# Kernel tuning notes

Measured on AMD Instinct MI355X. Metric: run time of the kernel, lower is better.

## Reference

```python
import jax, jax.numpy as jnp
import numpy as np

N_NODES = 50000
N_EDGES = 600000
DIMS = [128, 128, 128]  # input_dim + hidden_dims


def setup_inputs() -> dict:
    key = jax.random.key(0)
    ks = jax.random.split(key, 8)
    node_features = jax.random.normal(ks[0], (N_NODES, DIMS[0]), dtype=jnp.float32)
    edge_index = jax.random.randint(ks[1], (2, N_EDGES), 0, N_NODES, dtype=jnp.int64)
    # GCNConv params: weight [in, out] (glorot-ish), bias [out] (zeros init in PyG; use small randn)
    W1 = jax.random.normal(ks[2], (DIMS[0], DIMS[1]), dtype=jnp.float32) / np.sqrt(DIMS[0])
    b1 = jnp.zeros((DIMS[1],), dtype=jnp.float32)
    W2 = jax.random.normal(ks[3], (DIMS[1], DIMS[2]), dtype=jnp.float32) / np.sqrt(DIMS[1])
    b2 = jnp.zeros((DIMS[2],), dtype=jnp.float32)
    return {"node_features": node_features, "edge_index": edge_index,
            "W1": W1, "b1": b1, "W2": W2, "b2": b2}


def _gcn_norm(edge_index, n_nodes):
    # Add self loops, then symmetric normalization as in PyG gcn_norm.
    loop = jnp.arange(n_nodes, dtype=edge_index.dtype)
    src = jnp.concatenate([edge_index[0], loop])  # message sources (x_j)
    dst = jnp.concatenate([edge_index[1], loop])  # aggregation targets
    deg = jax.ops.segment_sum(jnp.ones_like(dst, dtype=jnp.float32), dst,
                              num_segments=n_nodes)
    dinv = jnp.where(deg > 0, jax.lax.rsqrt(jnp.maximum(deg, 1.0)), 0.0)
    norm = dinv[src] * dinv[dst]  # [E + N]
    return src, dst, norm


def _gcn_layer(x, W, b, src, dst, norm, n_nodes):
    h = x @ W                                  # [N, out]
    msgs = h[src] * norm[:, None]              # gather + scale  [E+N, out]
    out = jax.ops.segment_sum(msgs, dst, num_segments=n_nodes)  # scatter-add
    return out + b


def reference(node_features, edge_index, W1, b1, W2, b2):
    n_nodes = node_features.shape[0]
    src, dst, norm = _gcn_norm(edge_index, n_nodes)
    x = _gcn_layer(node_features, W1, b1, src, dst, norm, n_nodes)
    x = jax.nn.relu(x)  # ReLU between layers, none after last
    x = _gcn_layer(x, W2, b2, src, dst, norm, n_nodes)
    return x
```

## Files before the change

### kernel.cpp

```cpp
#include <hip/hip_runtime.h>
#include <hip/hip_bf16.h>

typedef __bf16 bf16_t;
typedef __bf16 bf16x8 __attribute__((ext_vector_type(8)));
typedef float f32x4 __attribute__((ext_vector_type(4)));
typedef unsigned short u16;

#define DIM 128
#define CAPE 62

__global__ void k_prep(const float* __restrict__ W1, const float* __restrict__ W2,
                       bf16_t* __restrict__ TH1, bf16_t* __restrict__ TL1,
                       bf16_t* __restrict__ TH2, bf16_t* __restrict__ TL2) {
    int b = blockIdx.x;
    const float* W = (b == 0) ? W1 : W2;
    bf16_t* TH = (b == 0) ? TH1 : TH2;
    bf16_t* TL = (b == 0) ? TL1 : TL2;
    for (int idx = threadIdx.x; idx < 128 * 128; idx += 256) {
        int j    = idx & 7;
        int lane = (idx >> 3) & 63;
        int kc   = (idx >> 9) & 3;
        int nt   = idx >> 11;
        int nn = nt * 16 + (lane & 15);
        int k  = kc * 32 + (lane >> 4) * 8 + j;
        float wv = W[k * 128 + nn];
        bf16_t h = (bf16_t)wv;
        TH[idx] = h;
        TL[idx] = (bf16_t)(wv - (float)h);
    }
}

__global__ __launch_bounds__(256) void k_front(
        const bf16_t* __restrict__ TH1, const bf16_t* __restrict__ TL1,
        const float* __restrict__ A, bf16_t* __restrict__ H, int M, int SB,
        const int* __restrict__ EI, int* __restrict__ ell, int e) {
    int b = blockIdx.x;
    int tid = threadIdx.x;
    if (b < SB) {
        __shared__ int any;
        if (tid == 0) any = 0;
        __syncthreads();
        long e0 = ((long)b * 256 + tid) * 8;
        long rem = (long)e - e0;
        int ns = rem >= 8 ? 8 : (rem > 0 ? (int)rem : 0);
        int s[8], d[8];
        int hi = 0;
        if (ns == 8) {
            int4 p0 = *(const int4*)(EI + 2 * e0);
            int4 p1 = *(const int4*)(EI + 2 * e0 + 4);
            int4 p2 = *(const int4*)(EI + 2 * e0 + 8);
            int4 p3 = *(const int4*)(EI + 2 * e0 + 12);
            s[0] = p0.x; s[1] = p0.z; s[2] = p1.x; s[3] = p1.z;
            s[4] = p2.x; s[5] = p2.z; s[6] = p3.x; s[7] = p3.z;
            hi = (p0.y | p0.w) | (p1.y | p1.w) | (p2.y | p2.w) | (p3.y | p3.w);
        } else {
            for (int q = 0; q < 8; q++) s[q] = 0;
            for (int q = 0; q < ns; q++) { s[q] = EI[2 * (e0 + q)]; hi |= EI[2 * (e0 + q) + 1]; }
        }
        if (hi) atomicOr(&any, 1);
        __syncthreads();
        for (int q = 0; q < 8; q++) d[q] = 0;
        if (any == 0) {
            if (ns == 8) {
                int4 q0 = *(const int4*)(EI + 2 * ((long)e + e0));
                int4 q1 = *(const int4*)(EI + 2 * ((long)e + e0) + 4);
                int4 q2 = *(const int4*)(EI + 2 * ((long)e + e0) + 8);
                int4 q3 = *(const int4*)(EI + 2 * ((long)e + e0) + 12);
                d[0] = q0.x; d[1] = q0.z; d[2] = q1.x; d[3] = q1.z;
                d[4] = q2.x; d[5] = q2.z; d[6] = q3.x; d[7] = q3.z;
            } else {
                for (int q = 0; q < ns; q++) d[q] = EI[2 * ((long)e + e0 + q)];
            }
        } else {
            if (ns == 8) {
                int4 s0 = *(const int4*)(EI + e0);
                int4 s1 = *(const int4*)(EI + e0 + 4);
                s[0] = s0.x; s[1] = s0.y; s[2] = s0.z; s[3] = s0.w;
                s[4] = s1.x; s[5] = s1.y; s[6] = s1.z; s[7] = s1.w;
                int4 d0 = *(const int4*)(EI + (long)e + e0);
                int4 d1 = *(const int4*)(EI + (long)e + e0 + 4);
                d[0] = d0.x; d[1] = d0.y; d[2] = d0.z; d[3] = d0.w;
                d[4] = d1.x; d[5] = d1.y; d[6] = d1.z; d[7] = d1.w;
            } else {
                for (int q = 0; q < ns; q++) { s[q] = EI[e0 + q]; d[q] = EI[(long)e + e0 + q]; }
            }
        }
        int pos[8];
#pragma unroll
        for (int q = 0; q < 8; q++)
            if (q < ns) pos[q] = atomicAdd(ell + (long)d[q] * 32 + 31, 1);
#pragma unroll
        for (int q = 0; q < 8; q++)
            if (q < ns && pos[q] < CAPE)
                ((u16*)ell)[(long)d[q] * 64 + pos[q]] = (u16)s[q];
        return;
    }
    int wave = tid >> 6, lane = tid & 63;
    long row_base = ((long)(b - SB) * 4 + wave) * 16;
    if (row_base >= M) return;
    int n16 = lane & 15, quad = lane >> 4;

    bf16x8 a_hi[4], a_lo[4];
    const float* arow = A + (row_base + n16) * DIM + quad * 8;
#pragma unroll
    for (int kc = 0; kc < 4; kc++) {
        float4 p0 = *(const float4*)(arow + kc * 32);
        float4 p1 = *(const float4*)(arow + kc * 32 + 4);
        float v[8] = {p0.x, p0.y, p0.z, p0.w, p1.x, p1.y, p1.z, p1.w};
#pragma unroll
        for (int j = 0; j < 8; j++) {
            bf16_t h = (bf16_t)v[j];
            a_hi[kc][j] = h;
            a_lo[kc][j] = (bf16_t)(v[j] - (float)h);
        }
    }
#pragma unroll
    for (int nt = 0; nt < 8; nt++) {
        f32x4 acc = {0.f, 0.f, 0.f, 0.f};
#pragma unroll
        for (int kc = 0; kc < 4; kc++) {
            long tb = ((long)(nt * 4 + kc) * 64 + lane) * 8;
            bf16x8 bh = *(const bf16x8*)(TH1 + tb);
            bf16x8 bl = *(const bf16x8*)(TL1 + tb);
            acc = __builtin_amdgcn_mfma_f32_16x16x32_bf16(a_hi[kc], bh, acc, 0, 0, 0);
            acc = __builtin_amdgcn_mfma_f32_16x16x32_bf16(a_lo[kc], bh, acc, 0, 0, 0);
            acc = __builtin_amdgcn_mfma_f32_16x16x32_bf16(a_hi[kc], bl, acc, 0, 0, 0);
        }
        bf16_t* hrow = H + (row_base + quad * 4) * DIM + nt * 16 + n16;
#pragma unroll
        for (int r = 0; r < 4; r++) hrow[(long)r * DIM] = (bf16_t)acc[r];
    }
}

__global__ void k_dinv(const int* __restrict__ ell, float* __restrict__ dinv, int n) {
    int g = blockIdx.x * 256 + threadIdx.x;
    if (g < n) dinv[g] = rsqrtf((float)(ell[(long)g * 32 + 31] + 1));
}

__global__ __launch_bounds__(256) void k_aggemm(const bf16_t* __restrict__ H,
        const int* __restrict__ ell, const float* __restrict__ dinv,
        const float* __restrict__ bias,
        const bf16_t* __restrict__ TH, const bf16_t* __restrict__ TL,
        bf16_t* __restrict__ H2, int n) {
    __shared__ bf16_t tile[16 * 128];
    __shared__ float sdinv[16];
    int lane = threadIdx.x & 63;
    int wave = threadIdx.x >> 6;
    int sub = lane >> 4;
    int sl  = lane & 15;
    int lr  = wave * 4 + sub;
    long i  = (long)blockIdx.x * 16 + lr;

    float d = dinv[i];
    int deg = ell[i * 32 + 31];
    if (deg > CAPE) deg = CAPE;
    const u16* crow = (const u16*)(ell + i * 32);
    float acc[8];
    {
        bf16x8 hs = *(const bf16x8*)(H + i * DIM + sl * 8);
#pragma unroll
        for (int q = 0; q < 8; q++) acc[q] = d * (float)hs[q];
    }
    ushort4 c0 = ((const ushort4*)crow)[0];
    ushort4 c1 = ((const ushort4*)crow)[1];
    ushort4 c2 = ((const ushort4*)crow)[2];
    ushort4 c3 = ((const ushort4*)crow)[3];
    u16 cols[16] = {c0.x, c0.y, c0.z, c0.w, c1.x, c1.y, c1.z, c1.w,
                    c2.x, c2.y, c2.z, c2.w, c3.x, c3.y, c3.z, c3.w};
    bf16x8 hv[16];
    float wv[16];
#pragma unroll
    for (int j = 0; j < 16; j++)
        if (j < deg) {
            int s0 = cols[j];
            wv[j] = dinv[s0];
            hv[j] = *(const bf16x8*)(H + (long)s0 * DIM + sl * 8);
        }
#pragma unroll
    for (int j = 0; j < 16; j++)
        if (j < deg) {
#pragma unroll
            for (int q = 0; q < 8; q++) acc[q] += wv[j] * (float)hv[j][q];
        }
    for (int j = 16; j < deg; j++) {
        int s0 = crow[j];
        float w0 = dinv[s0];
        bf16x8 h0 = *(const bf16x8*)(H + (long)s0 * DIM + sl * 8);
#pragma unroll
        for (int q = 0; q < 8; q++) acc[q] += w0 * (float)h0[q];
    }
    {
        float4 b0 = *(const float4*)(bias + sl * 8);
        float4 b1 = *(const float4*)(bias + sl * 8 + 4);
        float r[8];
        r[0] = d * acc[0] + b0.x; r[1] = d * acc[1] + b0.y;
        r[2] = d * acc[2] + b0.z; r[3] = d * acc[3] + b0.w;
        r[4] = d * acc[4] + b1.x; r[5] = d * acc[5] + b1.y;
        r[6] = d * acc[6] + b1.z; r[7] = d * acc[7] + b1.w;
        bf16x8 o;
#pragma unroll
        for (int q = 0; q < 8; q++) o[q] = (bf16_t)fmaxf(r[q], 0.f);
        int off = lr * 256 + ((sl * 16) ^ ((lr & 7) << 4));
        *(bf16x8*)((char*)tile + off) = o;
        if (sl == 0) sdinv[lr] = d;
    }
    __syncthreads();

    int n16 = sl, quad = sub;
    bf16x8 a[4];
#pragma unroll
    for (int kc = 0; kc < 4; kc++) {
        int off = n16 * 256 + (((kc * 64 + quad * 16)) ^ ((n16 & 7) << 4));
        a[kc] = *(const bf16x8*)((char*)tile + off);
    }
    float dr[4];
#pragma unroll
    for (int r = 0; r < 4; r++) dr[r] = sdinv[quad * 4 + r];
    long row_base = (long)blockIdx.x * 16;
#pragma unroll
    for (int t = 0; t < 2; t++) {
        int nt = wave * 2 + t;
        f32x4 acc2 = {0.f, 0.f, 0.f, 0.f};
#pragma unroll
        for (int kc = 0; kc < 4; kc++) {
            long tb = ((long)(nt * 4 + kc) * 64 + lane) * 8;
            bf16x8 bh = *(const bf16x8*)(TH + tb);
            bf16x8 bl = *(const bf16x8*)(TL + tb);
            acc2 = __builtin_amdgcn_mfma_f32_16x16x32_bf16(a[kc], bh, acc2, 0, 0, 0);
            acc2 = __builtin_amdgcn_mfma_f32_16x16x32_bf16(a[kc], bl, acc2, 0, 0, 0);
        }
        bf16_t* hrow = H2 + (row_base + quad * 4) * DIM + nt * 16 + n16;
#pragma unroll
        for (int r = 0; r < 4; r++) hrow[(long)r * DIM] = (bf16_t)(dr[r] * acc2[r]);
    }
}

__global__ __launch_bounds__(256) void k_agg2(const bf16_t* __restrict__ H,
        const int* __restrict__ ell, const float* __restrict__ dinv,
        const float* __restrict__ bias, float* __restrict__ outf, int n) {
    int lane = threadIdx.x & 63;
    int wave = threadIdx.x >> 6;
    int sub = lane >> 4;
    int sl  = lane & 15;
    long i = (long)(blockIdx.x * 4 + wave) * 4 + sub;
    if (i >= n) return;
    float d = dinv[i];
    int deg = ell[i * 32 + 31];
    if (deg > CAPE) deg = CAPE;
    const u16* crow = (const u16*)(ell + i * 32);
    float acc[8];
    {
        bf16x8 hs = *(const bf16x8*)(H + i * DIM + sl * 8);
#pragma unroll
        for (int q = 0; q < 8; q++) acc[q] = (float)hs[q];
    }
    ushort4 c0 = ((const ushort4*)crow)[0];
    ushort4 c1 = ((const ushort4*)crow)[1];
    ushort4 c2 = ((const ushort4*)crow)[2];
    ushort4 c3 = ((const ushort4*)crow)[3];
    u16 cols[16] = {c0.x, c0.y, c0.z, c0.w, c1.x, c1.y, c1.z, c1.w,
                    c2.x, c2.y, c2.z, c2.w, c3.x, c3.y, c3.z, c3.w};
    bf16x8 hv[16];
#pragma unroll
    for (int j = 0; j < 16; j++)
        if (j < deg) hv[j] = *(const bf16x8*)(H + (long)cols[j] * DIM + sl * 8);
#pragma unroll
    for (int j = 0; j < 16; j++)
        if (j < deg) {
#pragma unroll
            for (int q = 0; q < 8; q++) acc[q] += (float)hv[j][q];
        }
    for (int j = 16; j < deg; j++) {
        int s0 = crow[j];
        bf16x8 h0 = *(const bf16x8*)(H + (long)s0 * DIM + sl * 8);
#pragma unroll
        for (int q = 0; q < 8; q++) acc[q] += (float)h0[q];
    }
    {
        float4 b0 = *(const float4*)(bias + sl * 8);
        float4 b1 = *(const float4*)(bias + sl * 8 + 4);
        float* op = outf + i * DIM + sl * 8;
        *(float4*)op = make_float4(d * acc[0] + b0.x, d * acc[1] + b0.y,
                                   d * acc[2] + b0.z, d * acc[3] + b0.w);
        *(float4*)(op + 4) = make_float4(d * acc[4] + b1.x, d * acc[5] + b1.y,
                                         d * acc[6] + b1.z, d * acc[7] + b1.w);
    }
}

extern "C" void kernel_launch(void* const* d_in, const int* in_sizes, int n_in,
                              void* d_out, int out_size, void* d_ws, size_t ws_size,
                              hipStream_t stream) {
    const float* X  = (const float*)d_in[0];
    const int*   EI = (const int*)d_in[1];
    const float* W1 = (const float*)d_in[2];
    const float* B1 = (const float*)d_in[3];
    const float* W2 = (const float*)d_in[4];
    const float* B2 = (const float*)d_in[5];
    float* OUT = (float*)d_out;

    const int N = in_sizes[0] / DIM;
    const int E = in_sizes[1] / 2;
    (void)n_in; (void)out_size; (void)ws_size;

    char* w = (char*)d_ws;
    auto alloc = [&](size_t bytes) -> char* {
        char* p = w;
        w += (bytes + 255) & ~(size_t)255;
        return p;
    };
    int*    ell  = (int*)alloc((size_t)N * 128);
    float*  dinv = (float*)alloc((size_t)N * 4);
    bf16_t* TH1  = (bf16_t*)alloc(128 * 128 * 2);
    bf16_t* TL1  = (bf16_t*)alloc(128 * 128 * 2);
    bf16_t* TH2  = (bf16_t*)alloc(128 * 128 * 2);
    bf16_t* TL2  = (bf16_t*)alloc(128 * 128 * 2);
    bf16_t* H1   = (bf16_t*)alloc((size_t)N * DIM * 2);
    bf16_t* H2   = (bf16_t*)alloc((size_t)N * DIM * 2);

    int gN = (N + 255) / 256;
    int SB = (E + 2047) / 2048;
    int GB = (N + 63) / 64;
    int gT = (N + 15) / 16;

    hipMemsetAsync(ell, 0, (size_t)N * 128, stream);
    k_prep<<<2, 256, 0, stream>>>(W1, W2, TH1, TL1, TH2, TL2);
    k_front<<<SB + GB, 256, 0, stream>>>(TH1, TL1, X, H1, N, SB, EI, ell, E);
    k_dinv<<<gN, 256, 0, stream>>>(ell, dinv, N);
    k_aggemm<<<gT, 256, 0, stream>>>(H1, ell, dinv, B1, TH2, TL2, H2, N);
    k_agg2<<<gT, 256, 0, stream>>>(H2, ell, dinv, B2, OUT, N);
}
```

Baseline: 195.4 us.

## Partition ELL adjacency rows by source range into seven sub-buckets

Each destination row of the ELL adjacency is split into seven 32-byte sub-buckets selected by source id >> 13, each with its own atomic counter and capacity of 14. The aim is to spread atomic contention across several counters and to group neighbours by source range, so gathers from H hit nearby rows. Degree is now a sum of the seven counters. The ELL buffer doubles in size, so memset and reads cost more, and any sub-bucket holding more than 14 edges silently drops the extras, which risks wrong results for skewed degree distributions.

```diff
diff --git a/kernel.cpp b/kernel.cpp
--- a/kernel.cpp
+++ b/kernel.cpp
@@ -5,9 +5,12 @@
 typedef __bf16 bf16x8 __attribute__((ext_vector_type(8)));
 typedef float f32x4 __attribute__((ext_vector_type(4)));
 typedef unsigned short u16;
+typedef unsigned int u32;
 
 #define DIM 128
-#define CAPE 62
+#define SUBCAP 14
+#define PSHIFT 13
+#define NPART 7
 
 __global__ void k_prep(const float* __restrict__ W1, const float* __restrict__ W2,
                        bf16_t* __restrict__ TH1, bf16_t* __restrict__ TL1,
@@ -85,14 +88,18 @@
                 for (int q = 0; q < ns; q++) { s[q] = EI[e0 + q]; d[q] = EI[(long)e + e0 + q]; }
             }
         }
+        long bs[8];
         int pos[8];
 #pragma unroll
         for (int q = 0; q < 8; q++)
-            if (q < ns) pos[q] = atomicAdd(ell + (long)d[q] * 32 + 31, 1);
+            if (q < ns) {
+                bs[q] = (long)d[q] * 64 + (long)((s[q] >> PSHIFT) * 8);
+                pos[q] = atomicAdd(ell + bs[q], 1);
+            }
 #pragma unroll
         for (int q = 0; q < 8; q++)
-            if (q < ns && pos[q] < CAPE)
-                ((u16*)ell)[(long)d[q] * 64 + pos[q]] = (u16)s[q];
+            if (q < ns && pos[q] < SUBCAP)
+                ((u16*)ell)[bs[q] * 2 + 2 + pos[q]] = (u16)s[q];
         return;
     }
     int wave = tid >> 6, lane = tid & 63;
@@ -134,8 +141,22 @@
 
 __global__ void k_dinv(const int* __restrict__ ell, float* __restrict__ dinv, int n) {
     int g = blockIdx.x * 256 + threadIdx.x;
-    if (g < n) dinv[g] = rsqrtf((float)(ell[(long)g * 32 + 31] + 1));
-}
+    if (g < n) {
+        const int* row = ell + (long)g * 64;
+        int deg = 0;
+#pragma unroll
+        for (int p = 0; p < NPART; p++) deg += row[p * 8];
+        dinv[g] = rsqrtf((float)(deg + 1));
+    }
+}
+
+#define COL_A(a, j) ((int)(((j) == 0) ? ((a).y & 0xffff) : ((j) == 1) ? ((a).y >> 16) : \
+                           ((j) == 2) ? ((a).z & 0xffff) : ((j) == 3) ? ((a).z >> 16) : \
+                           ((j) == 4) ? ((a).w & 0xffff) : ((a).w >> 16)))
+#define COL_B(b, j2) ((int)(((j2) == 0) ? ((b).x & 0xffff) : ((j2) == 1) ? ((b).x >> 16) : \
+                            ((j2) == 2) ? ((b).y & 0xffff) : ((j2) == 3) ? ((b).y >> 16) : \
+                            ((j2) == 4) ? ((b).z & 0xffff) : ((j2) == 5) ? ((b).z >> 16) : \
+                            ((j2) == 6) ? ((b).w & 0xffff) : ((b).w >> 16)))
 
 __global__ __launch_bounds__(256) void k_aggemm(const bf16_t* __restrict__ H,
         const int* __restrict__ ell, const float* __restrict__ dinv,
@@ -152,42 +173,53 @@
     long i  = (long)blockIdx.x * 16 + lr;
 
     float d = dinv[i];
-    int deg = ell[i * 32 + 31];
-    if (deg > CAPE) deg = CAPE;
-    const u16* crow = (const u16*)(ell + i * 32);
+    const uint4* ru4 = (const uint4*)(ell + i * 64);
+    uint4 ra[NPART];
+#pragma unroll
+    for (int p = 0; p < NPART; p++) ra[p] = ru4[2 * p];
     float acc[8];
     {
         bf16x8 hs = *(const bf16x8*)(H + i * DIM + sl * 8);
 #pragma unroll
         for (int q = 0; q < 8; q++) acc[q] = d * (float)hs[q];
     }
-    ushort4 c0 = ((const ushort4*)crow)[0];
-    ushort4 c1 = ((const ushort4*)crow)[1];
-    ushort4 c2 = ((const ushort4*)crow)[2];
-    ushort4 c3 = ((const ushort4*)crow)[3];
-    u16 cols[16] = {c0.x, c0.y, c0.z, c0.w, c1.x, c1.y, c1.z, c1.w,
-                    c2.x, c2.y, c2.z, c2.w, c3.x, c3.y, c3.z, c3.w};
-    bf16x8 hv[16];
-    float wv[16];
-#pragma unroll
-    for (int j = 0; j < 16; j++)
-        if (j < deg) {
-            int s0 = cols[j];
-            wv[j] = dinv[s0];
-            hv[j] = *(const bf16x8*)(H + (long)s0 * DIM + sl * 8);
-        }
-#pragma unroll
-    for (int j = 0; j < 16; j++)
-        if (j < deg) {
-#pragma unroll
-            for (int q = 0; q < 8; q++) acc[q] += wv[j] * (float)hv[j][q];
-        }
-    for (int j = 16; j < deg; j++) {
-        int s0 = crow[j];
-        float w0 = dinv[s0];
-        bf16x8 h0 = *(const bf16x8*)(H + (long)s0 * DIM + sl * 8);
-#pragma unroll
-        for (int q = 0; q < 8; q++) acc[q] += w0 * (float)h0[q];
+#pragma unroll
+    for (int p = 0; p < NPART; p++) {
+        int dp = (int)ra[p].x;
+        if (dp > SUBCAP) dp = SUBCAP;
+        bf16x8 hv[6];
+        float wv[6];
+#pragma unroll
+        for (int j = 0; j < 6; j++)
+            if (j < dp) {
+                int s0 = COL_A(ra[p], j);
+                wv[j] = dinv[s0];
+                hv[j] = *(const bf16x8*)(H + (long)s0 * DIM + sl * 8);
+            }
+#pragma unroll
+        for (int j = 0; j < 6; j++)
+            if (j < dp) {
+#pragma unroll
+                for (int q = 0; q < 8; q++) acc[q] += wv[j] * (float)hv[j][q];
+            }
+        if (dp > 6) {
+            uint4 rb = ru4[2 * p + 1];
+            bf16x8 hv2[8];
+            float wv2[8];
+#pragma unroll
+            for (int j2 = 0; j2 < 8; j2++)
+                if (j2 + 6 < dp) {
+                    int s0 = COL_B(rb, j2);
+                    wv2[j2] = dinv[s0];
+                    hv2[j2] = *(const bf16x8*)(H + (long)s0 * DIM + sl * 8);
+                }
+#pragma unroll
+            for (int j2 = 0; j2 < 8; j2++)
+                if (j2 + 6 < dp) {
+#pragma unroll
+                    for (int q = 0; q < 8; q++) acc[q] += wv2[j2] * (float)hv2[j2][q];
+                }
+        }
     }
     {
         float4 b0 = *(const float4*)(bias + sl * 8);
@@ -245,36 +277,49 @@
     long i = (long)(blockIdx.x * 4 + wave) * 4 + sub;
     if (i >= n) return;
     float d = dinv[i];
-    int deg = ell[i * 32 + 31];
-    if (deg > CAPE) deg = CAPE;
-    const u16* crow = (const u16*)(ell + i * 32);
+    const uint4* ru4 = (const uint4*)(ell + i * 64);
+    uint4 ra[NPART];
+#pragma unroll
+    for (int p = 0; p < NPART; p++) ra[p] = ru4[2 * p];
     float acc[8];
     {
         bf16x8 hs = *(const bf16x8*)(H + i * DIM + sl * 8);
 #pragma unroll
         for (int q = 0; q < 8; q++) acc[q] = (float)hs[q];
     }
-    ushort4 c0 = ((const ushort4*)crow)[0];
-    ushort4 c1 = ((const ushort4*)crow)[1];
-    ushort4 c2 = ((const ushort4*)crow)[2];
-    ushort4 c3 = ((const ushort4*)crow)[3];
-    u16 cols[16] = {c0.x, c0.y, c0.z, c0.w, c1.x, c1.y, c1.z, c1.w,
-                    c2.x, c2.y, c2.z, c2.w, c3.x, c3.y, c3.z, c3.w};
-    bf16x8 hv[16];
-#pragma unroll
-    for (int j = 0; j < 16; j++)
-        if (j < deg) hv[j] = *(const bf16x8*)(H + (long)cols[j] * DIM + sl * 8);
-#pragma unroll
-    for (int j = 0; j < 16; j++)
-        if (j < deg) {
-#pragma unroll
-            for (int q = 0; q < 8; q++) acc[q] += (float)hv[j][q];
-        }
-    for (int j = 16; j < deg; j++) {
-        int s0 = crow[j];
-        bf16x8 h0 = *(const bf16x8*)(H + (long)s0 * DIM + sl * 8);
-#pragma unroll
-        for (int q = 0; q < 8; q++) acc[q] += (float)h0[q];
+#pragma unroll
+    for (int p = 0; p < NPART; p++) {
+        int dp = (int)ra[p].x;
+        if (dp > SUBCAP) dp = SUBCAP;
+        bf16x8 hv[6];
+#pragma unroll
+        for (int j = 0; j < 6; j++)
+            if (j < dp) {
+                int s0 = COL_A(ra[p], j);
+                hv[j] = *(const bf16x8*)(H + (long)s0 * DIM + sl * 8);
+            }
+#pragma unroll
+        for (int j = 0; j < 6; j++)
+            if (j < dp) {
+#pragma unroll
+                for (int q = 0; q < 8; q++) acc[q] += (float)hv[j][q];
+            }
+        if (dp > 6) {
+            uint4 rb = ru4[2 * p + 1];
+            bf16x8 hv2[8];
+#pragma unroll
+            for (int j2 = 0; j2 < 8; j2++)
+                if (j2 + 6 < dp) {
+                    int s0 = COL_B(rb, j2);
+                    hv2[j2] = *(const bf16x8*)(H + (long)s0 * DIM + sl * 8);
+                }
+#pragma unroll
+            for (int j2 = 0; j2 < 8; j2++)
+                if (j2 + 6 < dp) {
+#pragma unroll
+                    for (int q = 0; q < 8; q++) acc[q] += (float)hv2[j2][q];
+                }
+        }
     }
     {
         float4 b0 = *(const float4*)(bias + sl * 8);
@@ -308,7 +353,7 @@
         w += (bytes + 255) & ~(size_t)255;
         return p;
     };
-    int*    ell  = (int*)alloc((size_t)N * 128);
+    int*    ell  = (int*)alloc((size_t)N * 256);
     float*  dinv = (float*)alloc((size_t)N * 4);
     bf16_t* TH1  = (bf16_t*)alloc(128 * 128 * 2);
     bf16_t* TL1  = (bf16_t*)alloc(128 * 128 * 2);
@@ -322,7 +367,7 @@
     int GB = (N + 63) / 64;
     int gT = (N + 15) / 16;
 
-    hipMemsetAsync(ell, 0, (size_t)N * 128, stream);
+    hipMemsetAsync(ell, 0, (size_t)N * 256, stream);
     k_prep<<<2, 256, 0, stream>>>(W1, W2, TH1, TL1, TH2, TL2);
     k_front<<<SB + GB, 256, 0, stream>>>(TH1, TL1, X, H1, N, SB, EI, ell, E);
     k_dinv<<<gN, 256, 0, stream>>>(ell, dinv, N);
```

New measurement: 235.0 us. +20.3%, slower.

## Split feature matrices into 64-column halves to fit gathers in cache

Applied to the files above, without the earlier changes.

Stores H1 and H2 as two 64-column halves and runs each gather-aggregation pass over one half at a time, so each pass's randomly gathered working set (about 6.4 MB) is half as large and more likely to stay resident in cache. Layer-1 aggregation is split into a pass that writes the first half of the activations and a second pass that aggregates the other half, then runs the layer-2 GEMM from a shared tile. Layer-2 aggregation now takes two launches. Nontemporal stores are added for streaming outputs. The cost is extra launches, re-reading the ELL adjacency and dinv in every pass, and an extra round trip through memory for the intermediate half.

```diff
diff --git a/kernel.cpp b/kernel.cpp
--- a/kernel.cpp
+++ b/kernel.cpp
@@ -32,8 +32,8 @@
 
 __global__ __launch_bounds__(256) void k_front(
         const bf16_t* __restrict__ TH1, const bf16_t* __restrict__ TL1,
-        const float* __restrict__ A, bf16_t* __restrict__ H, int M, int SB,
-        const int* __restrict__ EI, int* __restrict__ ell, int e) {
+        const float* __restrict__ A, bf16_t* __restrict__ H1a, bf16_t* __restrict__ H1b,
+        int M, int SB, const int* __restrict__ EI, int* __restrict__ ell, int e) {
     int b = blockIdx.x;
     int tid = threadIdx.x;
     if (b < SB) {
@@ -126,9 +126,10 @@
             acc = __builtin_amdgcn_mfma_f32_16x16x32_bf16(a_lo[kc], bh, acc, 0, 0, 0);
             acc = __builtin_amdgcn_mfma_f32_16x16x32_bf16(a_hi[kc], bl, acc, 0, 0, 0);
         }
-        bf16_t* hrow = H + (row_base + quad * 4) * DIM + nt * 16 + n16;
-#pragma unroll
-        for (int r = 0; r < 4; r++) hrow[(long)r * DIM] = (bf16_t)acc[r];
+        bf16_t* base = (nt < 4) ? H1a : H1b;
+        long off = (row_base + quad * 4) * 64 + (nt & 3) * 16 + n16;
+#pragma unroll
+        for (int r = 0; r < 4; r++) base[off + (long)r * 64] = (bf16_t)acc[r];
     }
 }
 
@@ -137,27 +138,25 @@
     if (g < n) dinv[g] = rsqrtf((float)(ell[(long)g * 32 + 31] + 1));
 }
 
-__global__ __launch_bounds__(256) void k_aggemm(const bf16_t* __restrict__ H,
+__global__ __launch_bounds__(256) void k_agg1a(const bf16_t* __restrict__ Ha,
         const int* __restrict__ ell, const float* __restrict__ dinv,
-        const float* __restrict__ bias,
-        const bf16_t* __restrict__ TH, const bf16_t* __restrict__ TL,
-        bf16_t* __restrict__ H2, int n) {
-    __shared__ bf16_t tile[16 * 128];
-    __shared__ float sdinv[16];
+        const float* __restrict__ bias, bf16_t* __restrict__ outa, int n) {
     int lane = threadIdx.x & 63;
     int wave = threadIdx.x >> 6;
-    int sub = lane >> 4;
-    int sl  = lane & 15;
-    int lr  = wave * 4 + sub;
-    long i  = (long)blockIdx.x * 16 + lr;
-
-    float d = dinv[i];
-    int deg = ell[i * 32 + 31];
-    if (deg > CAPE) deg = CAPE;
-    const u16* crow = (const u16*)(ell + i * 32);
-    float acc[8];
-    {
-        bf16x8 hs = *(const bf16x8*)(H + i * DIM + sl * 8);
+    int g  = lane >> 3;
+    int sl = lane & 7;
+    long i = (long)blockIdx.x * 32 + wave * 8 + g;
+    bool act = (i < n);
+    float acc[8] = {0.f, 0.f, 0.f, 0.f, 0.f, 0.f, 0.f, 0.f};
+    float d = 0.f;
+    int deg = 0;
+    const u16* crow = (const u16*)ell;
+    if (act) {
+        d = dinv[i];
+        deg = ell[i * 32 + 31];
+        if (deg > CAPE) deg = CAPE;
+        crow = (const u16*)(ell + i * 32);
+        bf16x8 hs = *(const bf16x8*)(Ha + i * 64 + sl * 8);
 #pragma unroll
         for (int q = 0; q < 8; q++) acc[q] = d * (float)hs[q];
     }
@@ -174,7 +173,7 @@
         if (j < deg) {
             int s0 = cols[j];
             wv[j] = dinv[s0];
-            hv[j] = *(const bf16x8*)(H + (long)s0 * DIM + sl * 8);
+            hv[j] = *(const bf16x8*)(Ha + (long)s0 * 64 + sl * 8);
         }
 #pragma unroll
     for (int j = 0; j < 16; j++)
@@ -185,11 +184,11 @@
     for (int j = 16; j < deg; j++) {
         int s0 = crow[j];
         float w0 = dinv[s0];
-        bf16x8 h0 = *(const bf16x8*)(H + (long)s0 * DIM + sl * 8);
+        bf16x8 h0 = *(const bf16x8*)(Ha + (long)s0 * 64 + sl * 8);
 #pragma unroll
         for (int q = 0; q < 8; q++) acc[q] += w0 * (float)h0[q];
     }
-    {
+    if (act) {
         float4 b0 = *(const float4*)(bias + sl * 8);
         float4 b1 = *(const float4*)(bias + sl * 8 + 4);
         float r[8];
@@ -200,59 +199,36 @@
         bf16x8 o;
 #pragma unroll
         for (int q = 0; q < 8; q++) o[q] = (bf16_t)fmaxf(r[q], 0.f);
-        int off = lr * 256 + ((sl * 16) ^ ((lr & 7) << 4));
-        *(bf16x8*)((char*)tile + off) = o;
-        if (sl == 0) sdinv[lr] = d;
-    }
-    __syncthreads();
-
-    int n16 = sl, quad = sub;
-    bf16x8 a[4];
-#pragma unroll
-    for (int kc = 0; kc < 4; kc++) {
-        int off = n16 * 256 + (((kc * 64 + quad * 16)) ^ ((n16 & 7) << 4));
-        a[kc] = *(const bf16x8*)((char*)tile + off);
-    }
-    float dr[4];
-#pragma unroll
-    for (int r = 0; r < 4; r++) dr[r] = sdinv[quad * 4 + r];
-    long row_base = (long)blockIdx.x * 16;
-#pragma unroll
-    for (int t = 0; t < 2; t++) {
-        int nt = wave * 2 + t;
-        f32x4 acc2 = {0.f, 0.f, 0.f, 0.f};
-#pragma unroll
-        for (int kc = 0; kc < 4; kc++) {
-            long tb = ((long)(nt * 4 + kc) * 64 + lane) * 8;
-            bf16x8 bh = *(const bf16x8*)(TH + tb);
-            bf16x8 bl = *(const bf16x8*)(TL + tb);
-            acc2 = __builtin_amdgcn_mfma_f32_16x16x32_bf16(a[kc], bh, acc2, 0, 0, 0);
-            acc2 = __builtin_amdgcn_mfma_f32_16x16x32_bf16(a[kc], bl, acc2, 0, 0, 0);
-        }
-        bf16_t* hrow = H2 + (row_base + quad * 4) * DIM + nt * 16 + n16;
-#pragma unroll
-        for (int r = 0; r < 4; r++) hrow[(long)r * DIM] = (bf16_t)(dr[r] * acc2[r]);
-    }
-}
-
-__global__ __launch_bounds__(256) void k_agg2(const bf16_t* __restrict__ H,
+        __builtin_nontemporal_store(o, (bf16x8*)(outa + i * 64 + sl * 8));
+    }
+}
+
+__global__ __launch_bounds__(256) void k_agg1b(const bf16_t* __restrict__ Hb,
+        const bf16_t* __restrict__ X1a,
         const int* __restrict__ ell, const float* __restrict__ dinv,
-        const float* __restrict__ bias, float* __restrict__ outf, int n) {
+        const float* __restrict__ biasb,
+        const bf16_t* __restrict__ TH, const bf16_t* __restrict__ TL,
+        bf16_t* __restrict__ H2a, bf16_t* __restrict__ H2b, int n) {
+    __shared__ bf16_t tile[32 * 136];
     int lane = threadIdx.x & 63;
     int wave = threadIdx.x >> 6;
-    int sub = lane >> 4;
-    int sl  = lane & 15;
-    long i = (long)(blockIdx.x * 4 + wave) * 4 + sub;
-    if (i >= n) return;
-    float d = dinv[i];
-    int deg = ell[i * 32 + 31];
-    if (deg > CAPE) deg = CAPE;
-    const u16* crow = (const u16*)(ell + i * 32);
-    float acc[8];
-    {
-        bf16x8 hs = *(const bf16x8*)(H + i * DIM + sl * 8);
-#pragma unroll
-        for (int q = 0; q < 8; q++) acc[q] = (float)hs[q];
+    int g  = lane >> 3;
+    int sl = lane & 7;
+    int lr = wave * 8 + g;
+    long i = (long)blockIdx.x * 32 + lr;
+    bool act = (i < n);
+    float acc[8] = {0.f, 0.f, 0.f, 0.f, 0.f, 0.f, 0.f, 0.f};
+    float d = 0.f;
+    int deg = 0;
+    const u16* crow = (const u16*)ell;
+    if (act) {
+        d = dinv[i];
+        deg = ell[i * 32 + 31];
+        if (deg > CAPE) deg = CAPE;
+        crow = (const u16*)(ell + i * 32);
+        bf16x8 hs = *(const bf16x8*)(Hb + i * 64 + sl * 8);
+#pragma unroll
+        for (int q = 0; q < 8; q++) acc[q] = d * (float)hs[q];
     }
     ushort4 c0 = ((const ushort4*)crow)[0];
     ushort4 c1 = ((const ushort4*)crow)[1];
@@ -261,29 +237,135 @@
     u16 cols[16] = {c0.x, c0.y, c0.z, c0.w, c1.x, c1.y, c1.z, c1.w,
                     c2.x, c2.y, c2.z, c2.w, c3.x, c3.y, c3.z, c3.w};
     bf16x8 hv[16];
-#pragma unroll
-    for (int j = 0; j < 16; j++)
-        if (j < deg) hv[j] = *(const bf16x8*)(H + (long)cols[j] * DIM + sl * 8);
+    float wv[16];
 #pragma unroll
     for (int j = 0; j < 16; j++)
         if (j < deg) {
-#pragma unroll
-            for (int q = 0; q < 8; q++) acc[q] += (float)hv[j][q];
+            int s0 = cols[j];
+            wv[j] = dinv[s0];
+            hv[j] = *(const bf16x8*)(Hb + (long)s0 * 64 + sl * 8);
+        }
+#pragma unroll
+    for (int j = 0; j < 16; j++)
+        if (j < deg) {
+#pragma unroll
+            for (int q = 0; q < 8; q++) acc[q] += wv[j] * (float)hv[j][q];
         }
     for (int j = 16; j < deg; j++) {
         int s0 = crow[j];
-        bf16x8 h0 = *(const bf16x8*)(H + (long)s0 * DIM + sl * 8);
+        float w0 = dinv[s0];
+        bf16x8 h0 = *(const bf16x8*)(Hb + (long)s0 * 64 + sl * 8);
+#pragma unroll
+        for (int q = 0; q < 8; q++) acc[q] += w0 * (float)h0[q];
+    }
+    if (act) {
+        float4 b0 = *(const float4*)(biasb + sl * 8);
+        float4 b1 = *(const float4*)(biasb + sl * 8 + 4);
+        float r[8];
+        r[0] = d * acc[0] + b0.x; r[1] = d * acc[1] + b0.y;
+        r[2] = d * acc[2] + b0.z; r[3] = d * acc[3] + b0.w;
+        r[4] = d * acc[4] + b1.x; r[5] = d * acc[5] + b1.y;
+        r[6] = d * acc[6] + b1.z; r[7] = d * acc[7] + b1.w;
+        bf16x8 o;
+#pragma unroll
+        for (int q = 0; q < 8; q++) o[q] = (bf16_t)fmaxf(r[q], 0.f);
+        *(bf16x8*)(&tile[lr * 136 + 64 + sl * 8]) = o;
+        bf16x8 xa = __builtin_nontemporal_load((const bf16x8*)(X1a + i * 64 + sl * 8));
+        *(bf16x8*)(&tile[lr * 136 + sl * 8]) = xa;
+    }
+    __syncthreads();
+
+    int n16 = lane & 15, quad = lane >> 4;
+    int rt = wave >> 1;
+    int row = rt * 16 + n16;
+    long grow_base = (long)blockIdx.x * 32 + rt * 16;
+    bf16x8 a[4];
+#pragma unroll
+    for (int kc = 0; kc < 4; kc++)
+        a[kc] = *(const bf16x8*)(&tile[row * 136 + kc * 32 + quad * 8]);
+    float dr[4];
+#pragma unroll
+    for (int r = 0; r < 4; r++) {
+        long orow = grow_base + quad * 4 + r;
+        dr[r] = (orow < n) ? dinv[orow] : 0.f;
+    }
+#pragma unroll
+    for (int t = 0; t < 4; t++) {
+        int nt = (wave & 1) * 4 + t;
+        f32x4 acc2 = {0.f, 0.f, 0.f, 0.f};
+#pragma unroll
+        for (int kc = 0; kc < 4; kc++) {
+            long tb = ((long)(nt * 4 + kc) * 64 + lane) * 8;
+            bf16x8 bh = *(const bf16x8*)(TH + tb);
+            bf16x8 bl = *(const bf16x8*)(TL + tb);
+            acc2 = __builtin_amdgcn_mfma_f32_16x16x32_bf16(a[kc], bh, acc2, 0, 0, 0);
+            acc2 = __builtin_amdgcn_mfma_f32_16x16x32_bf16(a[kc], bl, acc2, 0, 0, 0);
+        }
+        bf16_t* base = (nt < 4) ? H2a : H2b;
+        int fo = (nt & 3) * 16 + n16;
+#pragma unroll
+        for (int r = 0; r < 4; r++) {
+            long orow = grow_base + quad * 4 + r;
+            if (orow < n)
+                __builtin_nontemporal_store((bf16_t)(dr[r] * acc2[r]), base + orow * 64 + fo);
+        }
+    }
+}
+
+__global__ __launch_bounds__(256) void k_agg2(const bf16_t* __restrict__ Hs,
+        const int* __restrict__ ell, const float* __restrict__ dinv,
+        const float* __restrict__ bias, float* __restrict__ outbase, int n) {
+    int lane = threadIdx.x & 63;
+    int wave = threadIdx.x >> 6;
+    int g  = lane >> 3;
+    int sl = lane & 7;
+    long i = (long)blockIdx.x * 32 + wave * 8 + g;
+    bool act = (i < n);
+    float acc[8] = {0.f, 0.f, 0.f, 0.f, 0.f, 0.f, 0.f, 0.f};
+    float d = 0.f;
+    int deg = 0;
+    const u16* crow = (const u16*)ell;
+    if (act) {
+        d = dinv[i];
+        deg = ell[i * 32 + 31];
+        if (deg > CAPE) deg = CAPE;
+        crow = (const u16*)(ell + i * 32);
+        bf16x8 hs = *(const bf16x8*)(Hs + i * 64 + sl * 8);
+#pragma unroll
+        for (int q = 0; q < 8; q++) acc[q] = (float)hs[q];
+    }
+    ushort4 c0 = ((const ushort4*)crow)[0];
+    ushort4 c1 = ((const ushort4*)crow)[1];
+    ushort4 c2 = ((const ushort4*)crow)[2];
+    ushort4 c3 = ((const ushort4*)crow)[3];
+    u16 cols[16] = {c0.x, c0.y, c0.z, c0.w, c1.x, c1.y, c1.z, c1.w,
+                    c2.x, c2.y, c2.z, c2.w, c3.x, c3.y, c3.z, c3.w};
+    bf16x8 hv[16];
+#pragma unroll
+    for (int j = 0; j < 16; j++)
+        if (j < deg) hv[j] = *(const bf16x8*)(Hs + (long)cols[j] * 64 + sl * 8);
+#pragma unroll
+    for (int j = 0; j < 16; j++)
+        if (j < deg) {
+#pragma unroll
+            for (int q = 0; q < 8; q++) acc[q] += (float)hv[j][q];
+        }
+    for (int j = 16; j < deg; j++) {
+        int s0 = crow[j];
+        bf16x8 h0 = *(const bf16x8*)(Hs + (long)s0 * 64 + sl * 8);
 #pragma unroll
         for (int q = 0; q < 8; q++) acc[q] += (float)h0[q];
     }
-    {
+    if (act) {
         float4 b0 = *(const float4*)(bias + sl * 8);
         float4 b1 = *(const float4*)(bias + sl * 8 + 4);
-        float* op = outf + i * DIM + sl * 8;
-        *(float4*)op = make_float4(d * acc[0] + b0.x, d * acc[1] + b0.y,
-                                   d * acc[2] + b0.z, d * acc[3] + b0.w);
-        *(float4*)(op + 4) = make_float4(d * acc[4] + b1.x, d * acc[5] + b1.y,
-                                         d * acc[6] + b1.z, d * acc[7] + b1.w);
+        float* op = outbase + i * 128 + sl * 8;
+        f32x4 o0 = {d * acc[0] + b0.x, d * acc[1] + b0.y,
+                    d * acc[2] + b0.z, d * acc[3] + b0.w};
+        f32x4 o1 = {d * acc[4] + b1.x, d * acc[5] + b1.y,
+                    d * acc[6] + b1.z, d * acc[7] + b1.w};
+        __builtin_nontemporal_store(o0, (f32x4*)op);
+        __builtin_nontemporal_store(o1, (f32x4*)(op + 4));
     }
 }
 
@@ -314,18 +396,23 @@
     bf16_t* TL1  = (bf16_t*)alloc(128 * 128 * 2);
     bf16_t* TH2  = (bf16_t*)alloc(128 * 128 * 2);
     bf16_t* TL2  = (bf16_t*)alloc(128 * 128 * 2);
-    bf16_t* H1   = (bf16_t*)alloc((size_t)N * DIM * 2);
-    bf16_t* H2   = (bf16_t*)alloc((size_t)N * DIM * 2);
-
-    int gN = (N + 255) / 256;
-    int SB = (E + 2047) / 2048;
-    int GB = (N + 63) / 64;
-    int gT = (N + 15) / 16;
+    bf16_t* H1a  = (bf16_t*)alloc((size_t)N * 64 * 2);
+    bf16_t* H1b  = (bf16_t*)alloc((size_t)N * 64 * 2);
+    bf16_t* X1a  = (bf16_t*)alloc((size_t)N * 64 * 2);
+    bf16_t* H2a  = (bf16_t*)alloc((size_t)N * 64 * 2);
+    bf16_t* H2b  = (bf16_t*)alloc((size_t)N * 64 * 2);
+
+    int gN  = (N + 255) / 256;
+    int SB  = (E + 2047) / 2048;
+    int GB  = (N + 63) / 64;
+    int gT  = (N + 31) / 32;
 
     hipMemsetAsync(ell, 0, (size_t)N * 128, stream);
     k_prep<<<2, 256, 0, stream>>>(W1, W2, TH1, TL1, TH2, TL2);
-    k_front<<<SB + GB, 256, 0, stream>>>(TH1, TL1, X, H1, N, SB, EI, ell, E);
+    k_front<<<SB + GB, 256, 0, stream>>>(TH1, TL1, X, H1a, H1b, N, SB, EI, ell, E);
     k_dinv<<<gN, 256, 0, stream>>>(ell, dinv, N);
-    k_aggemm<<<gT, 256, 0, stream>>>(H1, ell, dinv, B1, TH2, TL2, H2, N);
-    k_agg2<<<gT, 256, 0, stream>>>(H2, ell, dinv, B2, OUT, N);
-}
+    k_agg1a<<<gT, 256, 0, stream>>>(H1a, ell, dinv, B1, X1a, N);
+    k_agg1b<<<gT, 256, 0, stream>>>(H1b, X1a, ell, dinv, B1 + 64, TH2, TL2, H2a, H2b, N);
+    k_agg2<<<gT, 256, 0, stream>>>(H2a, ell, dinv, B2, OUT, N);
+    k_agg2<<<gT, 256, 0, stream>>>(H2b, ell, dinv, B2 + 64, OUT + 64, N);
+}
```

After: 219.4 us. +12.3%, slower.

## Build ELL adjacency via bucketed counting sort instead of global atomics

Applied to the files above, without the earlier changes.

Replaces per-edge global atomicAdd construction of the ELL adjacency with a two-pass bucketed counting sort. A histogram pass is fused into the first GEMM launch, followed by a single-block scan, a block-local scatter into destination buckets, and a per-bucket LDS build that writes ELL rows and dinv. The aim is to remove contended random global atomics and the memset of the ELL buffer. In exchange it adds three kernel launches, a serial single-block scan, and an extra edge buffer pass. The packing relies on node ids fitting 16 bits for sources and on dst>>8 fitting in the top byte.

```diff
diff --git a/kernel.cpp b/kernel.cpp
--- a/kernel.cpp
+++ b/kernel.cpp
@@ -5,9 +5,12 @@
 typedef __bf16 bf16x8 __attribute__((ext_vector_type(8)));
 typedef float f32x4 __attribute__((ext_vector_type(4)));
 typedef unsigned short u16;
+typedef unsigned int u32;
 
 #define DIM 128
 #define CAPE 62
+#define CHUNK 4096
+#define BSHIFT 8
 
 __global__ void k_prep(const float* __restrict__ W1, const float* __restrict__ W2,
                        bf16_t* __restrict__ TH1, bf16_t* __restrict__ TL1,
@@ -30,73 +33,44 @@
     }
 }
 
-__global__ __launch_bounds__(256) void k_front(
+__global__ __launch_bounds__(256) void k_hist_gemm(
         const bf16_t* __restrict__ TH1, const bf16_t* __restrict__ TL1,
-        const float* __restrict__ A, bf16_t* __restrict__ H, int M, int SB,
-        const int* __restrict__ EI, int* __restrict__ ell, int e) {
+        const float* __restrict__ A, bf16_t* __restrict__ H, int M, int HB,
+        const int* __restrict__ EI, int* __restrict__ hist, int NBUCK, int e) {
+    __shared__ int lhist[256];
+    __shared__ int any;
     int b = blockIdx.x;
     int tid = threadIdx.x;
-    if (b < SB) {
-        __shared__ int any;
+    if (b < HB) {
+        lhist[tid] = 0;
         if (tid == 0) any = 0;
         __syncthreads();
-        long e0 = ((long)b * 256 + tid) * 8;
-        long rem = (long)e - e0;
-        int ns = rem >= 8 ? 8 : (rem > 0 ? (int)rem : 0);
-        int s[8], d[8];
+        int base = b * CHUNK;
         int hi = 0;
-        if (ns == 8) {
-            int4 p0 = *(const int4*)(EI + 2 * e0);
-            int4 p1 = *(const int4*)(EI + 2 * e0 + 4);
-            int4 p2 = *(const int4*)(EI + 2 * e0 + 8);
-            int4 p3 = *(const int4*)(EI + 2 * e0 + 12);
-            s[0] = p0.x; s[1] = p0.z; s[2] = p1.x; s[3] = p1.z;
-            s[4] = p2.x; s[5] = p2.z; s[6] = p3.x; s[7] = p3.z;
-            hi = (p0.y | p0.w) | (p1.y | p1.w) | (p2.y | p2.w) | (p3.y | p3.w);
-        } else {
-            for (int q = 0; q < 8; q++) s[q] = 0;
-            for (int q = 0; q < ns; q++) { s[q] = EI[2 * (e0 + q)]; hi |= EI[2 * (e0 + q) + 1]; }
+#pragma unroll
+        for (int j = 0; j < 16; j++) {
+            int idx = base + j * 256 + tid;
+            if (idx < e) { int2 sv = *(const int2*)(EI + 2 * idx); hi |= sv.y; }
         }
         if (hi) atomicOr(&any, 1);
         __syncthreads();
-        for (int q = 0; q < 8; q++) d[q] = 0;
-        if (any == 0) {
-            if (ns == 8) {
-                int4 q0 = *(const int4*)(EI + 2 * ((long)e + e0));
-                int4 q1 = *(const int4*)(EI + 2 * ((long)e + e0) + 4);
-                int4 q2 = *(const int4*)(EI + 2 * ((long)e + e0) + 8);
-                int4 q3 = *(const int4*)(EI + 2 * ((long)e + e0) + 12);
-                d[0] = q0.x; d[1] = q0.z; d[2] = q1.x; d[3] = q1.z;
-                d[4] = q2.x; d[5] = q2.z; d[6] = q3.x; d[7] = q3.z;
-            } else {
-                for (int q = 0; q < ns; q++) d[q] = EI[2 * ((long)e + e0 + q)];
+        bool i64 = (any == 0);
+#pragma unroll
+        for (int j = 0; j < 16; j++) {
+            int idx = base + j * 256 + tid;
+            if (idx < e) {
+                int d;
+                if (i64) { int2 dv = *(const int2*)(EI + 2 * ((long)e + idx)); d = dv.x; }
+                else     { d = EI[e + idx]; }
+                atomicAdd(&lhist[d >> BSHIFT], 1);
             }
-        } else {
-            if (ns == 8) {
-                int4 s0 = *(const int4*)(EI + e0);
-                int4 s1 = *(const int4*)(EI + e0 + 4);
-                s[0] = s0.x; s[1] = s0.y; s[2] = s0.z; s[3] = s0.w;
-                s[4] = s1.x; s[5] = s1.y; s[6] = s1.z; s[7] = s1.w;
-                int4 d0 = *(const int4*)(EI + (long)e + e0);
-                int4 d1 = *(const int4*)(EI + (long)e + e0 + 4);
-                d[0] = d0.x; d[1] = d0.y; d[2] = d0.z; d[3] = d0.w;
-                d[4] = d1.x; d[5] = d1.y; d[6] = d1.z; d[7] = d1.w;
-            } else {
-                for (int q = 0; q < ns; q++) { s[q] = EI[e0 + q]; d[q] = EI[(long)e + e0 + q]; }
-            }
-        }
-        int pos[8];
-#pragma unroll
-        for (int q = 0; q < 8; q++)
-            if (q < ns) pos[q] = atomicAdd(ell + (long)d[q] * 32 + 31, 1);
-#pragma unroll
-        for (int q = 0; q < 8; q++)
-            if (q < ns && pos[q] < CAPE)
-                ((u16*)ell)[(long)d[q] * 64 + pos[q]] = (u16)s[q];
+        }
+        __syncthreads();
+        if (tid < NBUCK) hist[b * NBUCK + tid] = lhist[tid];
         return;
     }
     int wave = tid >> 6, lane = tid & 63;
-    long row_base = ((long)(b - SB) * 4 + wave) * 16;
+    long row_base = ((long)(b - HB) * 4 + wave) * 16;
     if (row_base >= M) return;
     int n16 = lane & 15, quad = lane >> 4;
 
@@ -132,9 +106,130 @@
     }
 }
 
-__global__ void k_dinv(const int* __restrict__ ell, float* __restrict__ dinv, int n) {
-    int g = blockIdx.x * 256 + threadIdx.x;
-    if (g < n) dinv[g] = rsqrtf((float)(ell[(long)g * 32 + 31] + 1));
+__global__ __launch_bounds__(256) void k_scan(const int* __restrict__ hist,
+        int* __restrict__ off, int* __restrict__ bstart, int HB, int NBUCK) {
+    __shared__ int T[256];
+    __shared__ int S[256];
+    int k = threadIdx.x;
+    int run = 0;
+    if (k < NBUCK) {
+        for (int b = 0; b < HB; b++) {
+            off[b * NBUCK + k] = run;
+            run += hist[b * NBUCK + k];
+        }
+    }
+    T[k] = run;
+    __syncthreads();
+    if (k == 0) {
+        int acc = 0;
+        for (int q = 0; q < NBUCK; q++) { S[q] = acc; acc += T[q]; }
+        bstart[NBUCK] = acc;
+    }
+    __syncthreads();
+    if (k < NBUCK) {
+        int s = S[k];
+        bstart[k] = s;
+        for (int b = 0; b < HB; b++) off[b * NBUCK + k] += s;
+    }
+}
+
+__global__ __launch_bounds__(256) void k_scatter(const int* __restrict__ EI,
+        const int* __restrict__ off, u32* __restrict__ ebuf, int NBUCK, int e) {
+    __shared__ u32 sedge[CHUNK];
+    __shared__ int ls[256];
+    __shared__ int lst[256];
+    __shared__ int cursor[256];
+    __shared__ int goff[256];
+    __shared__ int any;
+    int b = blockIdx.x;
+    int tid = threadIdx.x;
+    int base = b * CHUNK;
+    ls[tid] = 0;
+    if (tid == 0) any = 0;
+    __syncthreads();
+
+    int s[16], d[16];
+    int hi = 0;
+#pragma unroll
+    for (int j = 0; j < 16; j++) {
+        int idx = base + j * 256 + tid;
+        s[j] = 0; d[j] = 0;
+        if (idx < e) { int2 sv = *(const int2*)(EI + 2 * idx); s[j] = sv.x; hi |= sv.y; }
+    }
+    if (hi) atomicOr(&any, 1);
+    __syncthreads();
+    bool i64 = (any == 0);
+#pragma unroll
+    for (int j = 0; j < 16; j++) {
+        int idx = base + j * 256 + tid;
+        if (idx < e) {
+            if (i64) { int2 dv = *(const int2*)(EI + 2 * ((long)e + idx)); d[j] = dv.x; }
+            else     { s[j] = EI[idx]; d[j] = EI[e + idx]; }
+        }
+    }
+#pragma unroll
+    for (int j = 0; j < 16; j++) {
+        int idx = base + j * 256 + tid;
+        if (idx < e) atomicAdd(&ls[d[j] >> BSHIFT], 1);
+    }
+    if (tid < NBUCK) goff[tid] = off[b * NBUCK + tid];
+    __syncthreads();
+    for (int o = 1; o < 256; o <<= 1) {
+        int v = ls[tid];
+        if (tid >= o) v += ls[tid - o];
+        __syncthreads();
+        ls[tid] = v;
+        __syncthreads();
+    }
+    int ex = (tid == 0) ? 0 : ls[tid - 1];
+    lst[tid] = ex;
+    cursor[tid] = ex;
+    __syncthreads();
+#pragma unroll
+    for (int j = 0; j < 16; j++) {
+        int idx = base + j * 256 + tid;
+        if (idx < e) {
+            int k = d[j] >> BSHIFT;
+            int p = atomicAdd(&cursor[k], 1);
+            sedge[p] = (u32)(s[j] & 0xffff) | ((u32)d[j] << 16);
+        }
+    }
+    __syncthreads();
+    int total = ls[255];
+    for (int p = tid; p < total; p += 256) {
+        u32 ed = sedge[p];
+        int k = (int)(ed >> 24);
+        ebuf[goff[k] + (p - lst[k])] = ed;
+    }
+}
+
+__global__ __launch_bounds__(256) void k_ebuild(const u32* __restrict__ ebuf,
+        const int* __restrict__ bstart, int* __restrict__ ell,
+        float* __restrict__ dinv, int n) {
+    __shared__ u16 lell[256 * 64];
+    __shared__ int lcnt[256];
+    int k = blockIdx.x;
+    int tid = threadIdx.x;
+    lcnt[tid] = 0;
+    __syncthreads();
+    int lo = bstart[k], hix = bstart[k + 1];
+    for (int i = lo + tid; i < hix; i += 256) {
+        u32 ed = ebuf[i];
+        int d8 = (int)((ed >> 16) & 255);
+        int p = atomicAdd(&lcnt[d8], 1);
+        if (p < CAPE) lell[d8 * 64 + p] = (u16)(ed & 0xffff);
+    }
+    __syncthreads();
+    int node = k * 256 + tid;
+    if (node < n) {
+        int c = lcnt[tid];
+        ((int*)lell)[tid * 32 + 31] = c;
+        const int4* src = (const int4*)(lell + tid * 64);
+        int4* dst = (int4*)(ell + (long)node * 32);
+#pragma unroll
+        for (int q = 0; q < 8; q++) dst[q] = src[q];
+        dinv[node] = rsqrtf((float)(c + 1));
+    }
 }
 
 __global__ __launch_bounds__(256) void k_aggemm(const bf16_t* __restrict__ H,
@@ -280,10 +375,12 @@
         float4 b0 = *(const float4*)(bias + sl * 8);
         float4 b1 = *(const float4*)(bias + sl * 8 + 4);
         float* op = outf + i * DIM + sl * 8;
-        *(float4*)op = make_float4(d * acc[0] + b0.x, d * acc[1] + b0.y,
-                                   d * acc[2] + b0.z, d * acc[3] + b0.w);
-        *(float4*)(op + 4) = make_float4(d * acc[4] + b1.x, d * acc[5] + b1.y,
-                                         d * acc[6] + b1.z, d * acc[7] + b1.w);
+        f32x4 o0 = {d * acc[0] + b0.x, d * acc[1] + b0.y,
+                    d * acc[2] + b0.z, d * acc[3] + b0.w};
+        f32x4 o1 = {d * acc[4] + b1.x, d * acc[5] + b1.y,
+                    d * acc[6] + b1.z, d * acc[7] + b1.w};
+        *(f32x4*)op = o0;
+        *(f32x4*)(op + 4) = o1;
     }
 }
 
@@ -308,24 +405,30 @@
         w += (bytes + 255) & ~(size_t)255;
         return p;
     };
-    int*    ell  = (int*)alloc((size_t)N * 128);
-    float*  dinv = (float*)alloc((size_t)N * 4);
-    bf16_t* TH1  = (bf16_t*)alloc(128 * 128 * 2);
-    bf16_t* TL1  = (bf16_t*)alloc(128 * 128 * 2);
-    bf16_t* TH2  = (bf16_t*)alloc(128 * 128 * 2);
-    bf16_t* TL2  = (bf16_t*)alloc(128 * 128 * 2);
-    bf16_t* H1   = (bf16_t*)alloc((size_t)N * DIM * 2);
-    bf16_t* H2   = (bf16_t*)alloc((size_t)N * DIM * 2);
-
-    int gN = (N + 255) / 256;
-    int SB = (E + 2047) / 2048;
+    const int HB    = (E + CHUNK - 1) / CHUNK;
+    const int NBUCK = (N + 255) / 256;
+
+    int*    ell   = (int*)alloc((size_t)N * 128);
+    float*  dinv  = (float*)alloc((size_t)N * 4);
+    bf16_t* TH1   = (bf16_t*)alloc(128 * 128 * 2);
+    bf16_t* TL1   = (bf16_t*)alloc(128 * 128 * 2);
+    bf16_t* TH2   = (bf16_t*)alloc(128 * 128 * 2);
+    bf16_t* TL2   = (bf16_t*)alloc(128 * 128 * 2);
+    bf16_t* H1    = (bf16_t*)alloc((size_t)N * DIM * 2);
+    bf16_t* H2    = (bf16_t*)alloc((size_t)N * DIM * 2);
+    u32*    ebuf  = (u32*)alloc((size_t)E * 4);
+    int*    hist  = (int*)alloc((size_t)HB * NBUCK * 4);
+    int*    off   = (int*)alloc((size_t)HB * NBUCK * 4);
+    int*    bst   = (int*)alloc((size_t)(NBUCK + 1) * 4);
+
     int GB = (N + 63) / 64;
     int gT = (N + 15) / 16;
 
-    hipMemsetAsync(ell, 0, (size_t)N * 128, stream);
     k_prep<<<2, 256, 0, stream>>>(W1, W2, TH1, TL1, TH2, TL2);
-    k_front<<<SB + GB, 256, 0, stream>>>(TH1, TL1, X, H1, N, SB, EI, ell, E);
-    k_dinv<<<gN, 256, 0, stream>>>(ell, dinv, N);
+    k_hist_gemm<<<HB + GB, 256, 0, stream>>>(TH1, TL1, X, H1, N, HB, EI, hist, NBUCK, E);
+    k_scan<<<1, 256, 0, stream>>>(hist, off, bst, HB, NBUCK);
+    k_scatter<<<HB, 256, 0, stream>>>(EI, off, ebuf, NBUCK, E);
+    k_ebuild<<<NBUCK, 256, 0, stream>>>(ebuf, bst, ell, dinv, N);
     k_aggemm<<<gT, 256, 0, stream>>>(H1, ell, dinv, B1, TH2, TL2, H2, N);
     k_agg2<<<gT, 256, 0, stream>>>(H2, ell, dinv, B2, OUT, N);
 }
```

After: 264.7 us. 35.4% more time.
